# Optimization experiments

Measured on AMD Instinct MI355X. Metric: run time of the kernel, lower is better.

## Reference

```python
import jax, jax.numpy as jnp
import numpy as np
import math

B, S, HID, NH = 2, 2048, 1024, 16
HD = HID // NH


def setup_inputs() -> dict:
    key = jax.random.key(0)
    ks = jax.random.split(key, 6)
    scale = 0.02
    return {
        "hidden_states": jax.random.normal(ks[0], (B, S, HID), dtype=jnp.float32),
        "attention_mask": jnp.ones((B, S), dtype=jnp.float32),
        "Wq": jax.random.normal(ks[1], (HID, HID), dtype=jnp.float32) * scale,
        "bq": jnp.zeros((HID,), dtype=jnp.float32),
        "Wk": jax.random.normal(ks[2], (HID, HID), dtype=jnp.float32) * scale,
        "bk": jnp.zeros((HID,), dtype=jnp.float32),
        "Wv": jax.random.normal(ks[3], (HID, HID), dtype=jnp.float32) * scale,
        "bv": jnp.zeros((HID,), dtype=jnp.float32),
        "Wo": jax.random.normal(ks[4], (HID, HID), dtype=jnp.float32) * scale,
        "bo": jnp.zeros((HID,), dtype=jnp.float32),
        "beta": jnp.zeros((1,), dtype=jnp.float32),
        "gamma": jnp.ones((1,), dtype=jnp.float32),
    }


def reference(hidden_states, attention_mask, Wq, bq, Wk, bk, Wv, bv, Wo, bo, beta, gamma):
    b, s, h = hidden_states.shape

    def proj(W, bias):
        # torch Linear: x @ W.T + b ; then split heads -> [B, NH, S, HD]
        y = jnp.einsum('bsh,oh->bso', hidden_states, W) + bias
        return y.reshape(b, s, NH, HD).transpose(0, 2, 1, 3)

    q = proj(Wq, bq)
    k = proj(Wk, bk)
    v = proj(Wv, bv)

    scores = jnp.einsum('bnsd,bntd->bnst', q, k) / math.sqrt(HD)  # [B,NH,S,S]
    # extended mask: [B,1,1,S]; additive -1e4 on masked positions
    scores = scores + (1.0 - attention_mask)[:, None, None, :] * (-10000.0)

    # ConsMax: exp(scores - beta - rowmax) / gamma (no sum normalization)
    shifted = scores - beta
    shifted = shifted - jnp.max(shifted, axis=-1, keepdims=True)
    probs = jnp.exp(shifted) / gamma  # dropout p=0 -> identity

    ctx = jnp.einsum('bnst,bntd->bnsd', probs, v)  # [B,NH,S,HD]
    ctx = ctx.transpose(0, 2, 1, 3).reshape(b, s, h)
    return jnp.einsum('bsh,oh->bso', ctx, Wo) + bo
```

## Files before the change

### kernel.cpp

```cpp
#include <hip/hip_runtime.h>
#include <hip/hip_bf16.h>


typedef unsigned short u16;
typedef __attribute__((ext_vector_type(8))) short short8;
typedef __attribute__((ext_vector_type(4))) float floatx4;

constexpr int B_  = 2;
constexpr int S_  = 2048;
constexpr int HID = 1024;
constexpr int NH  = 16;
constexpr int HD  = 64;
constexpr int M_  = B_ * S_;

constexpr float LOG2E   = 1.4426950408889634f;
constexpr float QSCALE  = 0.125f * LOG2E;
constexpr float MSCALE  = -10000.0f * LOG2E;

__device__ __forceinline__ u16 f2us(float f) {
    union { float f; unsigned int i; } x;
    x.f = f;
    unsigned int r = x.i + 0x7FFFu + ((x.i >> 16) & 1u);
    return (u16)(r >> 16);
}
__device__ __forceinline__ unsigned pk2(float a, float b) {
    __hip_bfloat162 h = __float22bfloat162_rn(make_float2(a, b));
    unsigned u; __builtin_memcpy(&u, &h, 4); return u;
}
__device__ __forceinline__ void async_lds16(const u16* g, u16* l) {
    __builtin_amdgcn_global_load_lds(
        (const __attribute__((address_space(1))) unsigned int*)g,
        (__attribute__((address_space(3))) unsigned int*)l, 16, 0, 0);
}

__global__ __launch_bounds__(256)
void cvt_all(const float* __restrict__ hs, const float* __restrict__ Wq,
             const float* __restrict__ Wk, const float* __restrict__ Wv,
             const float* __restrict__ Wo,
             u16* __restrict__ hs_bf, u16* __restrict__ Wcat,
             u16* __restrict__ Wo_bf)
{
    const int bid = blockIdx.x;
    const float* src;
    u16* dst;
    size_t base;
    if (bid < 4096) {
        src = hs; dst = hs_bf; base = (size_t)bid * 1024;
    } else if (bid < 7168) {
        const int s = (bid - 4096) >> 10;
        src = (s == 0) ? Wq : (s == 1) ? Wk : Wv;
        dst = Wcat + (size_t)s * 1048576;
        base = (size_t)((bid - 4096) & 1023) * 1024;
    } else {
        src = Wo; dst = Wo_bf; base = (size_t)(bid - 7168) * 1024;
    }
    const size_t i = base + threadIdx.x * 4;
    float4 t = *(const float4*)(src + i);
    uint2 o = { pk2(t.x, t.y), pk2(t.z, t.w) };
    *(uint2*)(dst + i) = o;
}

__global__ __launch_bounds__(256)
void qkv_gemm(const u16* __restrict__ hs_bf, const u16* __restrict__ Wcat,
              const float* __restrict__ bq, const float* __restrict__ bk,
              const float* __restrict__ bv,
              u16* __restrict__ Qo, u16* __restrict__ Ko, u16* __restrict__ VT)
{
    __shared__ u16 Alds[8192];
    __shared__ u16 Blds[8192];

    const int tid = threadIdx.x;
    const int id  = blockIdx.x;
    const int xcd = id & 7, jb = id >> 3;
    const int m0  = (xcd * 4 + (jb & 3)) * 128;
    const int n0g = (jb >> 2) * 128;
    const int p   = n0g >> 10;
    const int n0  = n0g & 1023;
    const u16*   Wb = Wcat + (size_t)p * 1048576;
    const float* bi = (p == 0) ? bq : (p == 1) ? bk : bv;
    const float  osc = (p == 0) ? QSCALE : 1.0f;

    const int w = tid >> 6, l = tid & 63;
    const int quad = l >> 4, l16 = l & 15;
    const int wy = w >> 1, wx = w & 1;

    floatx4 acc[4][4];
    #pragma unroll
    for (int i = 0; i < 4; ++i)
        #pragma unroll
        for (int j = 0; j < 4; ++j) acc[i][j] = (floatx4){0.f, 0.f, 0.f, 0.f};

    for (int k0 = 0; k0 < HID; k0 += 64) {
        __syncthreads();
        #pragma unroll
        for (int c = 0; c < 2; ++c) {
            const int s = w * 2 + c;
            #pragma unroll
            for (int t = 0; t < 2; ++t) {
                async_lds16(hs_bf + (size_t)(m0 + s * 16 + l16) * HID + k0 + t * 32 + quad * 8,
                            &Alds[s * 1024 + t * 512]);
                async_lds16(Wb + (size_t)(n0 + s * 16 + l16) * HID + k0 + t * 32 + quad * 8,
                            &Blds[s * 1024 + t * 512]);
            }
        }
        __syncthreads();

        #pragma unroll
        for (int t = 0; t < 2; ++t) {
            short8 afr[4], bfr[4];
            #pragma unroll
            for (int i = 0; i < 4; ++i)
                afr[i] = *(const short8*)&Alds[(wy*4 + i) * 1024 + t * 512 + l * 8];
            #pragma unroll
            for (int j = 0; j < 4; ++j)
                bfr[j] = *(const short8*)&Blds[(wx*4 + j) * 1024 + t * 512 + l * 8];
            #pragma unroll
            for (int i = 0; i < 4; ++i)
                #pragma unroll
                for (int j = 0; j < 4; ++j)
                    acc[i][j] = __builtin_amdgcn_mfma_f32_16x16x32_bf16(afr[i], bfr[j], acc[i][j], 0, 0, 0);
        }
    }

    #pragma unroll
    for (int i = 0; i < 4; ++i)
        #pragma unroll
        for (int j = 0; j < 4; ++j) {
            const int nn   = n0 + wx * 64 + j * 16 + l16;
            const int head = nn >> 6, dd = nn & 63;
            const float bb_ = bi[nn];
            const int mmb = m0 + wy * 64 + i * 16 + quad * 4;
            const int b = mmb >> 11, ss = mmb & (S_ - 1);
            if (p == 2) {
                uint2 st = { pk2(acc[i][j][0] + bb_, acc[i][j][1] + bb_),
                             pk2(acc[i][j][2] + bb_, acc[i][j][3] + bb_) };
                *(uint2*)(VT + (((size_t)(b * NH + head)) * HD + dd) * S_ + ss) = st;
            } else {
                u16* Out = (p == 0) ? Qo : Ko;
                #pragma unroll
                for (int rg = 0; rg < 4; ++rg)
                    Out[(((size_t)b * NH + head) * S_ + ss + rg) * HD + dd] =
                        f2us((acc[i][j][rg] + bb_) * osc);
            }
        }
}

__global__ __launch_bounds__(256, 2)
void attn7(const u16* __restrict__ Qg, const u16* __restrict__ Kg,
           const u16* __restrict__ VTg, const float* __restrict__ mask,
           const float* __restrict__ gamma, u16* __restrict__ ctx)
{
    __shared__ u16 Kb[8192];
    __shared__ u16 Vb[8192];
    __shared__ u16 Pb[16384];

    const int tid = threadIdx.x;
    const int w = tid >> 6, l = tid & 63;
    const int quad = l >> 4, l16 = l & 15;
    const int id  = blockIdx.x;
    const int xcd = id & 7, jb = id >> 3;
    const int bh  = xcd * 4 + (jb >> 4);
    const int qb  = jb & 15;
    const int b0  = bh >> 4, h = bh & (NH - 1);

    const u16* Qb    = Qg  + (size_t)bh * S_ * HD;
    const u16* Kbg   = Kg  + (size_t)bh * S_ * HD;
    const u16* Vbg   = VTg + (size_t)bh * HD * S_;
    const float* mG  = mask + (size_t)b0 * S_;

    short8 qf[2][2];
    #pragma unroll
    for (int u = 0; u < 2; ++u)
        #pragma unroll
        for (int t = 0; t < 2; ++t)
            qf[u][t] = *(const short8*)(Qb + ((size_t)qb * 128 + 32 * w + u * 16 + l16) * HD + 32 * t + quad * 8);

    floatx4 o_acc[2][4];
    #pragma unroll
    for (int u = 0; u < 2; ++u)
        #pragma unroll
        for (int jn = 0; jn < 4; ++jn) o_acc[u][jn] = (floatx4){0.f, 0.f, 0.f, 0.f};
    float m_run[2] = { -1e30f, -1e30f };

    u16* Pw = Pb + w * 4096;

    for (int kt = 0; kt < S_ / 128; ++kt) {
        __syncthreads();
        #pragma unroll
        for (int c = 0; c < 2; ++c) {
            const int s = w * 2 + c;
            #pragma unroll
            for (int t = 0; t < 2; ++t)
                async_lds16(Kbg + ((size_t)kt * 128 + s * 16 + l16) * HD + t * 32 + quad * 8,
                            &Kb[s * 1024 + t * 512]);
        }
        #pragma unroll
        for (int tt = 0; tt < 4; ++tt)
            async_lds16(Vbg + (size_t)(w * 16 + l16) * S_ + kt * 128 + tt * 32 + quad * 8,
                        &Vb[w * 2048 + tt * 512]);
        __syncthreads();

        float4 mv[8];
        #pragma unroll
        for (int j = 0; j < 8; ++j) {
            float4 r = *(const float4*)(mG + kt * 128 + j * 16 + quad * 4);
            mv[j].x = (1.0f - r.x) * MSCALE;
            mv[j].y = (1.0f - r.y) * MSCALE;
            mv[j].z = (1.0f - r.z) * MSCALE;
            mv[j].w = (1.0f - r.w) * MSCALE;
        }

        #pragma unroll
        for (int j = 0; j < 8; ++j) {
            short8 kf0 = *(const short8*)&Kb[j * 1024 + l * 8];
            short8 kf1 = *(const short8*)&Kb[j * 1024 + 512 + l * 8];
            floatx4 s0 = (floatx4){0.f, 0.f, 0.f, 0.f};
            floatx4 s1 = (floatx4){0.f, 0.f, 0.f, 0.f};
            s0 = __builtin_amdgcn_mfma_f32_16x16x32_bf16(kf0, qf[0][0], s0, 0, 0, 0);
            s0 = __builtin_amdgcn_mfma_f32_16x16x32_bf16(kf1, qf[0][1], s0, 0, 0, 0);
            s1 = __builtin_amdgcn_mfma_f32_16x16x32_bf16(kf0, qf[1][0], s1, 0, 0, 0);
            s1 = __builtin_amdgcn_mfma_f32_16x16x32_bf16(kf1, qf[1][1], s1, 0, 0, 0);
            s0[0] += mv[j].x; s0[1] += mv[j].y; s0[2] += mv[j].z; s0[3] += mv[j].w;
            s1[0] += mv[j].x; s1[1] += mv[j].y; s1[2] += mv[j].z; s1[3] += mv[j].w;
            m_run[0] = fmaxf(fmaxf(fmaxf(s0[0], s0[1]), fmaxf(s0[2], s0[3])), m_run[0]);
            m_run[1] = fmaxf(fmaxf(fmaxf(s1[0], s1[1]), fmaxf(s1[2], s1[3])), m_run[1]);
            uint2 p0 = { pk2(exp2f(s0[0]), exp2f(s0[1])), pk2(exp2f(s0[2]), exp2f(s0[3])) };
            uint2 p1 = { pk2(exp2f(s1[0]), exp2f(s1[1])), pk2(exp2f(s1[2]), exp2f(s1[3])) };
            const int off = (j >> 1) * 512
                          + (l16 + 16 * ((j & 1) * 2 + (quad >> 1))) * 8
                          + (quad & 1) * 4;
            *(uint2*)&Pw[off]        = p0;
            *(uint2*)&Pw[2048 + off] = p1;
        }

        #pragma unroll
        for (int tt = 0; tt < 4; ++tt) {
            short8 pf0 = *(const short8*)&Pw[tt * 512 + l * 8];
            short8 pf1 = *(const short8*)&Pw[2048 + tt * 512 + l * 8];
            #pragma unroll
            for (int jn = 0; jn < 4; ++jn) {
                short8 vf = *(const short8*)&Vb[jn * 2048 + tt * 512 + l * 8];
                o_acc[0][jn] = __builtin_amdgcn_mfma_f32_16x16x32_bf16(pf0, vf, o_acc[0][jn], 0, 0, 0);
                o_acc[1][jn] = __builtin_amdgcn_mfma_f32_16x16x32_bf16(pf1, vf, o_acc[1][jn], 0, 0, 0);
            }
        }
    }

    const float ig = 1.0f / gamma[0];
    #pragma unroll
    for (int u = 0; u < 2; ++u) {
        float mx = m_run[u];
        mx = fmaxf(mx, __shfl_xor(mx, 16, 64));
        mx = fmaxf(mx, __shfl_xor(mx, 32, 64));
        #pragma unroll
        for (int i = 0; i < 4; ++i) {
            const float si = exp2f(-__shfl(mx, quad * 4 + i, 64)) * ig;
            const int srow = qb * 128 + 32 * w + u * 16 + quad * 4 + i;
            #pragma unroll
            for (int jn = 0; jn < 4; ++jn)
                ctx[((size_t)(b0 * S_ + srow)) * HID + h * HD + jn * 16 + l16] =
                    f2us(o_acc[u][jn][i] * si);
        }
    }
}

__global__ __launch_bounds__(256)
void out_gemm(const u16* __restrict__ ctx, const u16* __restrict__ Wo_bf,
              const float* __restrict__ bo, float* __restrict__ out)
{
    __shared__ u16 Alds[8192];
    __shared__ u16 Blds[4096];

    const int tid = threadIdx.x;
    const int id  = blockIdx.x;
    const int xcd = id & 7, jb = id >> 3;
    const int m0  = (xcd * 4 + (jb & 3)) * 128;
    const int n0  = (jb >> 2) * 64;

    const int w = tid >> 6, l = tid & 63;
    const int quad = l >> 4, l16 = l & 15;

    floatx4 acc[2][4];
    #pragma unroll
    for (int i = 0; i < 2; ++i)
        #pragma unroll
        for (int j = 0; j < 4; ++j) acc[i][j] = (floatx4){0.f, 0.f, 0.f, 0.f};

    for (int k0 = 0; k0 < HID; k0 += 64) {
        __syncthreads();
        #pragma unroll
        for (int c = 0; c < 2; ++c) {
            const int s = w * 2 + c;
            #pragma unroll
            for (int t = 0; t < 2; ++t)
                async_lds16(ctx + (size_t)(m0 + s * 16 + l16) * HID + k0 + t * 32 + quad * 8,
                            &Alds[s * 1024 + t * 512]);
        }
        #pragma unroll
        for (int t = 0; t < 2; ++t)
            async_lds16(Wo_bf + (size_t)(n0 + w * 16 + l16) * HID + k0 + t * 32 + quad * 8,
                        &Blds[w * 1024 + t * 512]);
        __syncthreads();

        #pragma unroll
        for (int t = 0; t < 2; ++t) {
            short8 afr[2], bfr[4];
            #pragma unroll
            for (int i = 0; i < 2; ++i)
                afr[i] = *(const short8*)&Alds[(w*2 + i) * 1024 + t * 512 + l * 8];
            #pragma unroll
            for (int j = 0; j < 4; ++j)
                bfr[j] = *(const short8*)&Blds[j * 1024 + t * 512 + l * 8];
            #pragma unroll
            for (int i = 0; i < 2; ++i)
                #pragma unroll
                for (int j = 0; j < 4; ++j)
                    acc[i][j] = __builtin_amdgcn_mfma_f32_16x16x32_bf16(afr[i], bfr[j], acc[i][j], 0, 0, 0);
        }
    }

    #pragma unroll
    for (int i = 0; i < 2; ++i)
        #pragma unroll
        for (int j = 0; j < 4; ++j) {
            const int nn = n0 + j * 16 + l16;
            const float bb_ = bo[nn];
            #pragma unroll
            for (int rg = 0; rg < 4; ++rg) {
                const int mm = m0 + w * 32 + i * 16 + quad * 4 + rg;
                out[(size_t)mm * HID + nn] = acc[i][j][rg] + bb_;
            }
        }
}

extern "C" void kernel_launch(void* const* d_in, const int* in_sizes, int n_in,
                              void* d_out, int out_size, void* d_ws, size_t ws_size,
                              hipStream_t stream)
{
    const float* hs    = (const float*)d_in[0];
    const float* mask  = (const float*)d_in[1];
    const float* Wq    = (const float*)d_in[2];
    const float* bq    = (const float*)d_in[3];
    const float* Wk    = (const float*)d_in[4];
    const float* bk    = (const float*)d_in[5];
    const float* Wv    = (const float*)d_in[6];
    const float* bv    = (const float*)d_in[7];
    const float* Wo    = (const float*)d_in[8];
    const float* bo    = (const float*)d_in[9];
    const float* gamma = (const float*)d_in[11];
    float* out = (float*)d_out;

    const size_t tsz = (size_t)B_ * NH * S_ * HD;
    u16* q     = (u16*)d_ws;
    u16* vT    = q + tsz;
    u16* Wcat  = vT + tsz;
    u16* Wo_bf = Wcat + 3u * 1048576u;
    u16* ctx   = Wo_bf + 1048576u;
    u16* hs_bf = (u16*)d_out;
    u16* kbuf  = hs_bf + tsz;

    cvt_all<<<dim3(8192), 256, 0, stream>>>(hs, Wq, Wk, Wv, Wo, hs_bf, Wcat, Wo_bf);
    qkv_gemm<<<dim3(768), 256, 0, stream>>>(hs_bf, Wcat, bq, bk, bv, q, kbuf, vT);
    attn7<<<dim3(512), 256, 0, stream>>>(q, kbuf, vT, mask, gamma, ctx);
    out_gemm<<<dim3(512), 256, 0, stream>>>(ctx, Wo_bf, bo, out);
}
```

Measured before the change: 259.0 us.

## Rewrite attention kernel with 32x32x16 MFMA, 64-key tiles and swizzled P buffer

```diff
diff --git a/kernel.cpp b/kernel.cpp
--- a/kernel.cpp
+++ b/kernel.cpp
@@ -5,17 +5,23 @@
 typedef unsigned short u16;
 typedef __attribute__((ext_vector_type(8))) short short8;
 typedef __attribute__((ext_vector_type(4))) float floatx4;
+typedef __attribute__((ext_vector_type(16))) float floatx16;
 
 constexpr int B_  = 2;
 constexpr int S_  = 2048;
 constexpr int HID = 1024;
 constexpr int NH  = 16;
 constexpr int HD  = 64;
-constexpr int M_  = B_ * S_;
 
 constexpr float LOG2E   = 1.4426950408889634f;
 constexpr float QSCALE  = 0.125f * LOG2E;
 constexpr float MSCALE  = -10000.0f * LOG2E;
+
+#if __has_builtin(__builtin_amdgcn_exp2f)
+#define EXP2(x) __builtin_amdgcn_exp2f(x)
+#else
+#define EXP2(x) exp2f(x)
+#endif
 
 __device__ __forceinline__ u16 f2us(float f) {
     union { float f; unsigned int i; } x;
@@ -145,18 +151,19 @@
         }
 }
 
-__global__ __launch_bounds__(256, 2)
-void attn7(const u16* __restrict__ Qg, const u16* __restrict__ Kg,
-           const u16* __restrict__ VTg, const float* __restrict__ mask,
-           const float* __restrict__ gamma, u16* __restrict__ ctx)
-{
-    __shared__ u16 Kb[8192];
-    __shared__ u16 Vb[8192];
-    __shared__ u16 Pb[16384];
+__global__ __launch_bounds__(256, 4)
+void attn10(const u16* __restrict__ Qg, const u16* __restrict__ Kg,
+            const u16* __restrict__ VTg, const float* __restrict__ mask,
+            const float* __restrict__ gamma, u16* __restrict__ ctx)
+{
+    __shared__ u16 Kb[4096];
+    __shared__ u16 Vb[4096];
+    __shared__ u16 Pq[8192];
 
     const int tid = threadIdx.x;
     const int w = tid >> 6, l = tid & 63;
-    const int quad = l >> 4, l16 = l & 15;
+    const int l32 = l & 31, hh = l >> 5;
+    const int swz = (l32 & 7) << 3;
     const int id  = blockIdx.x;
     const int xcd = id & 7, jb = id >> 3;
     const int bh  = xcd * 4 + (jb >> 4);
@@ -168,100 +175,88 @@
     const u16* Vbg   = VTg + (size_t)bh * HD * S_;
     const float* mG  = mask + (size_t)b0 * S_;
 
-    short8 qf[2][2];
-    #pragma unroll
-    for (int u = 0; u < 2; ++u)
-        #pragma unroll
-        for (int t = 0; t < 2; ++t)
-            qf[u][t] = *(const short8*)(Qb + ((size_t)qb * 128 + 32 * w + u * 16 + l16) * HD + 32 * t + quad * 8);
-
-    floatx4 o_acc[2][4];
-    #pragma unroll
-    for (int u = 0; u < 2; ++u)
-        #pragma unroll
-        for (int jn = 0; jn < 4; ++jn) o_acc[u][jn] = (floatx4){0.f, 0.f, 0.f, 0.f};
-    float m_run[2] = { -1e30f, -1e30f };
-
-    u16* Pw = Pb + w * 4096;
-
-    for (int kt = 0; kt < S_ / 128; ++kt) {
+    const int qrow = qb * 128 + w * 32 + l32;
+
+    short8 qB[4];
+    #pragma unroll
+    for (int dc = 0; dc < 4; ++dc)
+        qB[dc] = *(const short8*)(Qb + (size_t)qrow * HD + dc * 16 + hh * 8);
+
+    floatx16 oacc[2];
+    #pragma unroll
+    for (int db = 0; db < 2; ++db)
+        #pragma unroll
+        for (int i = 0; i < 16; ++i) oacc[db][i] = 0.f;
+    float m_run = -1e30f;
+
+    u16* Pw = Pq + w * 2048;
+
+    for (int kt = 0; kt < S_ / 64; ++kt) {
         __syncthreads();
         #pragma unroll
         for (int c = 0; c < 2; ++c) {
-            const int s = w * 2 + c;
-            #pragma unroll
-            for (int t = 0; t < 2; ++t)
-                async_lds16(Kbg + ((size_t)kt * 128 + s * 16 + l16) * HD + t * 32 + quad * 8,
-                            &Kb[s * 1024 + t * 512]);
-        }
-        #pragma unroll
-        for (int tt = 0; tt < 4; ++tt)
-            async_lds16(Vbg + (size_t)(w * 16 + l16) * S_ + kt * 128 + tt * 32 + quad * 8,
-                        &Vb[w * 2048 + tt * 512]);
-        __syncthreads();
-
-        float4 mv[8];
-        #pragma unroll
-        for (int j = 0; j < 8; ++j) {
-            float4 r = *(const float4*)(mG + kt * 128 + j * 16 + quad * 4);
-            mv[j].x = (1.0f - r.x) * MSCALE;
-            mv[j].y = (1.0f - r.y) * MSCALE;
-            mv[j].z = (1.0f - r.z) * MSCALE;
-            mv[j].w = (1.0f - r.w) * MSCALE;
-        }
-
-        #pragma unroll
-        for (int j = 0; j < 8; ++j) {
-            short8 kf0 = *(const short8*)&Kb[j * 1024 + l * 8];
-            short8 kf1 = *(const short8*)&Kb[j * 1024 + 512 + l * 8];
-            floatx4 s0 = (floatx4){0.f, 0.f, 0.f, 0.f};
-            floatx4 s1 = (floatx4){0.f, 0.f, 0.f, 0.f};
-            s0 = __builtin_amdgcn_mfma_f32_16x16x32_bf16(kf0, qf[0][0], s0, 0, 0, 0);
-            s0 = __builtin_amdgcn_mfma_f32_16x16x32_bf16(kf1, qf[0][1], s0, 0, 0, 0);
-            s1 = __builtin_amdgcn_mfma_f32_16x16x32_bf16(kf0, qf[1][0], s1, 0, 0, 0);
-            s1 = __builtin_amdgcn_mfma_f32_16x16x32_bf16(kf1, qf[1][1], s1, 0, 0, 0);
-            s0[0] += mv[j].x; s0[1] += mv[j].y; s0[2] += mv[j].z; s0[3] += mv[j].w;
-            s1[0] += mv[j].x; s1[1] += mv[j].y; s1[2] += mv[j].z; s1[3] += mv[j].w;
-            m_run[0] = fmaxf(fmaxf(fmaxf(s0[0], s0[1]), fmaxf(s0[2], s0[3])), m_run[0]);
-            m_run[1] = fmaxf(fmaxf(fmaxf(s1[0], s1[1]), fmaxf(s1[2], s1[3])), m_run[1]);
-            uint2 p0 = { pk2(exp2f(s0[0]), exp2f(s0[1])), pk2(exp2f(s0[2]), exp2f(s0[3])) };
-            uint2 p1 = { pk2(exp2f(s1[0]), exp2f(s1[1])), pk2(exp2f(s1[2]), exp2f(s1[3])) };
-            const int off = (j >> 1) * 512
-                          + (l16 + 16 * ((j & 1) * 2 + (quad >> 1))) * 8
-                          + (quad & 1) * 4;
-            *(uint2*)&Pw[off]        = p0;
-            *(uint2*)&Pw[2048 + off] = p1;
-        }
-
-        #pragma unroll
-        for (int tt = 0; tt < 4; ++tt) {
-            short8 pf0 = *(const short8*)&Pw[tt * 512 + l * 8];
-            short8 pf1 = *(const short8*)&Pw[2048 + tt * 512 + l * 8];
-            #pragma unroll
-            for (int jn = 0; jn < 4; ++jn) {
-                short8 vf = *(const short8*)&Vb[jn * 2048 + tt * 512 + l * 8];
-                o_acc[0][jn] = __builtin_amdgcn_mfma_f32_16x16x32_bf16(pf0, vf, o_acc[0][jn], 0, 0, 0);
-                o_acc[1][jn] = __builtin_amdgcn_mfma_f32_16x16x32_bf16(pf1, vf, o_acc[1][jn], 0, 0, 0);
+            const int r = w * 2 + c;
+            const int kb = r >> 2, dc = r & 3;
+            async_lds16(Kbg + (size_t)(kt * 64 + kb * 32 + l32) * HD + dc * 16 + hh * 8,
+                        &Kb[r * 512]);
+            const int db = r >> 2, kg = r & 3;
+            async_lds16(Vbg + (size_t)(db * 32 + l32) * S_ + kt * 64 + kg * 16 + hh * 8,
+                        &Vb[r * 512]);
+        }
+        __syncthreads();
+
+        #pragma unroll
+        for (int kb = 0; kb < 2; ++kb) {
+            const float* mrow = mG + kt * 64 + kb * 32 + 4 * hh;
+            floatx16 acc;
+            #pragma unroll
+            for (int g = 0; g < 4; ++g) {
+                float4 mv = *(const float4*)(mrow + g * 8);
+                acc[4*g]   = fmaf(mv.x, -MSCALE, MSCALE);
+                acc[4*g+1] = fmaf(mv.y, -MSCALE, MSCALE);
+                acc[4*g+2] = fmaf(mv.z, -MSCALE, MSCALE);
+                acc[4*g+3] = fmaf(mv.w, -MSCALE, MSCALE);
+            }
+            #pragma unroll
+            for (int dc = 0; dc < 4; ++dc) {
+                short8 kf = *(const short8*)&Kb[(kb * 4 + dc) * 512 + l * 8];
+                acc = __builtin_amdgcn_mfma_f32_32x32x16_bf16(kf, qB[dc], acc, 0, 0, 0);
+            }
+            float mr = m_run;
+            #pragma unroll
+            for (int i = 0; i < 16; ++i) mr = fmaxf(mr, acc[i]);
+            m_run = mr;
+            #pragma unroll
+            for (int g = 0; g < 4; ++g) {
+                uint2 pw = { pk2(EXP2(acc[4*g]),   EXP2(acc[4*g+1])),
+                             pk2(EXP2(acc[4*g+2]), EXP2(acc[4*g+3])) };
+                const int koff = kb * 32 + 8 * g + 4 * hh;
+                *(uint2*)&Pw[l32 * 64 + (koff ^ swz)] = pw;
+            }
+        }
+
+        #pragma unroll
+        for (int kg = 0; kg < 4; ++kg) {
+            short8 pf = *(const short8*)&Pw[l32 * 64 + ((kg * 16 + hh * 8) ^ swz)];
+            #pragma unroll
+            for (int db = 0; db < 2; ++db) {
+                short8 vf = *(const short8*)&Vb[(db * 4 + kg) * 512 + l * 8];
+                oacc[db] = __builtin_amdgcn_mfma_f32_32x32x16_bf16(vf, pf, oacc[db], 0, 0, 0);
             }
         }
     }
 
-    const float ig = 1.0f / gamma[0];
-    #pragma unroll
-    for (int u = 0; u < 2; ++u) {
-        float mx = m_run[u];
-        mx = fmaxf(mx, __shfl_xor(mx, 16, 64));
-        mx = fmaxf(mx, __shfl_xor(mx, 32, 64));
-        #pragma unroll
-        for (int i = 0; i < 4; ++i) {
-            const float si = exp2f(-__shfl(mx, quad * 4 + i, 64)) * ig;
-            const int srow = qb * 128 + 32 * w + u * 16 + quad * 4 + i;
-            #pragma unroll
-            for (int jn = 0; jn < 4; ++jn)
-                ctx[((size_t)(b0 * S_ + srow)) * HID + h * HD + jn * 16 + l16] =
-                    f2us(o_acc[u][jn][i] * si);
-        }
-    }
+    const float mx = fmaxf(m_run, __shfl_xor(m_run, 32, 64));
+    const float si = EXP2(-mx) * (1.0f / gamma[0]);
+    u16* crow = ctx + (size_t)(b0 * S_ + qrow) * HID + h * HD;
+    #pragma unroll
+    for (int db = 0; db < 2; ++db)
+        #pragma unroll
+        for (int g = 0; g < 4; ++g) {
+            uint2 st = { pk2(oacc[db][g * 4 + 0] * si, oacc[db][g * 4 + 1] * si),
+                         pk2(oacc[db][g * 4 + 2] * si, oacc[db][g * 4 + 3] * si) };
+            *(uint2*)(crow + db * 32 + g * 8 + hh * 4) = st;
+        }
 }
 
 __global__ __launch_bounds__(256)
@@ -361,6 +356,6 @@
 
     cvt_all<<<dim3(8192), 256, 0, stream>>>(hs, Wq, Wk, Wv, Wo, hs_bf, Wcat, Wo_bf);
     qkv_gemm<<<dim3(768), 256, 0, stream>>>(hs_bf, Wcat, bq, bk, bv, q, kbuf, vT);
-    attn7<<<dim3(512), 256, 0, stream>>>(q, kbuf, vT, mask, gamma, ctx);
+    attn10<<<dim3(512), 256, 0, stream>>>(q, kbuf, vT, mask, gamma, ctx);
     out_gemm<<<dim3(512), 256, 0, stream>>>(ctx, Wo_bf, bo, out);
 }
```

After: 250.6 us. 1.03x faster.
